# Performance work log

Hardware: AMD Instinct MI355X
Metric: run time of the kernel (lower is better)

Reference implementation:

```python
import jax, jax.numpy as jnp
import numpy as np

B, P, ENC, DEC, ATT, EMB, V, MEM, TCAP = 64, 196, 2048, 512, 512, 512, 10000, 128, 22
T = TCAP - 1  # max decode length (caption_lengths - 1)


def setup_inputs() -> dict:
    key = jax.random.key(0)
    ks = iter(jax.random.split(key, 32))
    def w(shape, s=0.02):
        return (jax.random.normal(next(ks), shape, jnp.float32) * s)
    encoder_out = jax.random.normal(next(ks), (B, P, ENC), jnp.float32)
    encoded_captions = jax.random.randint(next(ks), (B, TCAP), 0, V)
    lens = np.sort(np.asarray(jax.random.randint(next(ks), (B,), 5, TCAP + 1)))[::-1].copy()
    lens[0] = TCAP  # ensure max(decode_lengths) == T
    caption_lengths = jnp.asarray(lens, jnp.int32)
    return {
        'encoder_out': encoder_out,
        'encoded_captions': encoded_captions,
        'caption_lengths': caption_lengths,
        'emb_table': w((V, EMB), 0.05),
        # Linear weights stored as [in, out] (torch W.T), so y = x @ W + b
        'W_enc': w((ENC, ATT)), 'b_enc': jnp.zeros((ATT,), jnp.float32),
        'W_dec': w((DEC, ATT)), 'b_dec': jnp.zeros((ATT,), jnp.float32),
        'W_full': w((ATT, 1)), 'b_full': jnp.zeros((1,), jnp.float32),
        'W_inith': w((ENC, DEC)), 'b_inith': jnp.zeros((DEC,), jnp.float32),
        'W_initc': w((ENC, DEC)), 'b_initc': jnp.zeros((DEC,), jnp.float32),
        'W_beta': w((DEC, ENC)), 'b_beta': jnp.zeros((ENC,), jnp.float32),
        # LSTMCell (torch gate order i, f, g, o), stored as [in, 4*dec]
        'W_ih': w((EMB + ENC, 4 * DEC)), 'b_ih': jnp.zeros((4 * DEC,), jnp.float32),
        'W_hh': w((DEC, 4 * DEC)), 'b_hh': jnp.zeros((4 * DEC,), jnp.float32),
        'memory_bank': jax.random.normal(next(ks), (MEM, DEC), jnp.float32),
        'W_fc': w((DEC, V)), 'b_fc': jnp.zeros((V,), jnp.float32),
    }


def _decode(encoder_out, encoded_captions, caption_lengths, emb_table,
            W_enc, b_enc, W_dec, b_dec, W_full, b_full,
            W_inith, b_inith, W_initc, b_initc, W_beta, b_beta,
            W_ih, b_ih, W_hh, b_hh, memory_bank, W_fc, b_fc):
    dec_len = caption_lengths - 1  # decode_lengths
    embs = emb_table[encoded_captions]                 # [B, TCAP, EMB]
    mean_enc = encoder_out.mean(axis=1)                # [B, ENC]
    h0 = mean_enc @ W_inith + b_inith
    c0 = mean_enc @ W_initc + b_initc
    att1 = encoder_out @ W_enc + b_enc                 # [B, P, ATT] precomputed

    x_seq = jnp.swapaxes(embs[:, :T, :], 0, 1)         # [T, B, EMB]
    mask_seq = jnp.arange(T)[:, None] < dec_len[None, :]  # [T, B]

    def step(carry, inp):
        h, c = carry
        x_t, m = inp                                   # [B,EMB], [B]
        # attention
        att2 = h @ W_dec + b_dec                       # [B, ATT]
        e = (jax.nn.relu(att1 + att2[:, None, :]) @ W_full)[..., 0] + b_full[0]  # [B, P]
        alpha = jax.nn.softmax(e, axis=1)
        awe = jnp.einsum('bpe,bp->be', encoder_out, alpha)  # [B, ENC]
        gate = jax.nn.sigmoid(h @ W_beta + b_beta)
        awe = gate * awe
        # LSTMCell
        xi = jnp.concatenate([x_t, awe], axis=1)
        gates = xi @ W_ih + b_ih + h @ W_hh + b_hh      # [B, 4*DEC]
        gi, gf, gg, go = jnp.split(gates, 4, axis=1)
        c_new = jax.nn.sigmoid(gf) * c + jax.nn.sigmoid(gi) * jnp.tanh(gg)
        h_new = jax.nn.sigmoid(go) * jnp.tanh(c_new)
        # hash memory
        sim = h_new @ memory_bank.T                    # [B, MEM]
        h_new = h_new + jax.nn.softmax(sim, axis=1) @ memory_bank
        # fc (dropout = identity in eval)
        preds = h_new @ W_fc + b_fc                    # [B, V]
        m2 = m[:, None]
        h = jnp.where(m2, h_new, h)
        c = jnp.where(m2, c_new, c)
        preds = jnp.where(m2, preds, 0.0)
        alpha = jnp.where(m2, alpha, 0.0)
        return (h, c), (preds, alpha)

    (_, _), (preds_seq, alpha_seq) = jax.lax.scan(step, (h0, c0), (x_seq, mask_seq))
    predictions = jnp.swapaxes(preds_seq, 0, 1)        # [B, T, V]
    alphas = jnp.swapaxes(alpha_seq, 0, 1)             # [B, T, P]
    return predictions, dec_len, alphas


def reference(encoder_out, encoded_captions, caption_lengths, emb_table,
              W_enc, b_enc, W_dec, b_dec, W_full, b_full,
              W_inith, b_inith, W_initc, b_initc, W_beta, b_beta,
              W_ih, b_ih, W_hh, b_hh, memory_bank, W_fc, b_fc):
    return _decode(encoder_out, encoded_captions, caption_lengths, emb_table,
                   W_enc, b_enc, W_dec, b_dec, W_full, b_full,
                   W_inith, b_inith, W_initc, b_initc, W_beta, b_beta,
                   W_ih, b_ih, W_hh, b_hh, memory_bank, W_fc, b_fc)
```

## Files before the change

### kernel.cpp

```cpp
#include <hip/hip_runtime.h>

#define BB   64
#define PP   196
#define ENCD 2048
#define DECD 512
#define VV   10000
#define TT   21
#define KIH  2560

typedef __attribute__((ext_vector_type(8))) short bf16x8;
typedef __attribute__((ext_vector_type(4))) float f32x4;
typedef float f32x2 __attribute__((ext_vector_type(2)));

__device__ __forceinline__ float sigm(float x)   { return 1.f / (1.f + __expf(-x)); }
__device__ __forceinline__ float tanh_f(float x) { return 1.f - 2.f / (1.f + __expf(2.f * x)); }
__device__ __forceinline__ ushort f2bf(float x) {
    unsigned u = __float_as_uint(x);
    unsigned r = (u + 0x7FFFu + ((u >> 16) & 1u)) >> 16;
    return (ushort)r;
}
__device__ __forceinline__ float bf2f(ushort u) {
    return __uint_as_float(((unsigned)u) << 16);
}
union U8 { float4 f4; ushort u[8]; };

#if __has_builtin(__builtin_amdgcn_cvt_pk_fp8_f32) && __has_builtin(__builtin_amdgcn_cvt_pk_f32_fp8)
#define HAVE_HW_FP8 1
#endif

__device__ uint enc8m(float x) {
    uint s = (__float_as_uint(x) >> 31) << 7;
    float ax = fabsf(x);
    if (!(ax > 0.f)) return s;
    if (ax >= 448.f) return s | 0x7e;
    int e; float m = frexpf(ax, &e);
    int E = e - 1 + 7;
    if (E <= 0) { int q = (int)rintf(ax * 512.f); if (q > 7) return s | 0x08; return s | (uint)q; }
    int q = (int)rintf((m * 2.f - 1.f) * 8.f);
    if (q == 8) { q = 0; ++E; if (E > 15) return s | 0x7e; }
    return s | ((uint)E << 3) | (uint)q;
}
__device__ __forceinline__ float dec8m(uint b) {
    uint s = b >> 7, e = (b >> 3) & 15, m = b & 7;
    float v = (e == 0) ? (float)m * (1.f / 512.f) : ldexpf(1.f + (float)m * 0.125f, (int)e - 7);
    return s ? -v : v;
}
__device__ __forceinline__ uint pkfp8x4(float a, float b, float c, float d) {
#ifdef HAVE_HW_FP8
    int v = __builtin_amdgcn_cvt_pk_fp8_f32(a, b, 0, false);
    v = __builtin_amdgcn_cvt_pk_fp8_f32(c, d, v, true);
    return (uint)v;
#else
    return enc8m(a) | (enc8m(b) << 8) | (enc8m(c) << 16) | (enc8m(d) << 24);
#endif
}
__device__ __forceinline__ void dec8x4(uint v, float out[4]) {
#ifdef HAVE_HW_FP8
    f32x2 lo = __builtin_amdgcn_cvt_pk_f32_fp8((int)v, false);
    f32x2 hi = __builtin_amdgcn_cvt_pk_f32_fp8((int)v, true);
    out[0] = lo[0]; out[1] = lo[1]; out[2] = hi[0]; out[3] = hi[1];
#else
    out[0] = dec8m(v & 255); out[1] = dec8m((v >> 8) & 255);
    out[2] = dec8m((v >> 16) & 255); out[3] = dec8m(v >> 24);
#endif
}


__global__ void k_cvt(const float* __restrict__ in, ushort* __restrict__ out, int n4) {
    int i = blockIdx.x * 256 + threadIdx.x;
    if (i >= n4) return;
    float4 v = ((const float4*)in)[i];
    ushort4 o; o.x = f2bf(v.x); o.y = f2bf(v.y); o.z = f2bf(v.z); o.w = f2bf(v.w);
    ((ushort4*)out)[i] = o;
}

__global__ void k_cvt8(const float* __restrict__ in, uint* __restrict__ out, int n4) {
    int i = blockIdx.x * 256 + threadIdx.x;
    if (i >= n4) return;
    float4 v = ((const float4*)in)[i];
    out[i] = pkfp8x4(v.x, v.y, v.z, v.w);
}

__global__ void k_mean16(const ushort* __restrict__ encB, float* __restrict__ mean) {
    int idx = blockIdx.x * 256 + threadIdx.x;
    int b = idx >> 10, e2 = idx & 1023;
    const uint* p = (const uint*)encB + (size_t)b * PP * 1024 + e2;
    float s0 = 0.f, s1 = 0.f;
    #pragma unroll 7
    for (int i = 0; i < PP; ++i) {
        uint v = p[(size_t)i * 1024];
        s0 += __uint_as_float(v << 16);
        s1 += __uint_as_float(v & 0xffff0000u);
    }
    mean[b * 2048 + e2 * 2]     = s0 * (1.f / 196.f);
    mean[b * 2048 + e2 * 2 + 1] = s1 * (1.f / 196.f);
}

__global__ __launch_bounds__(256) void k_ipart(const float* __restrict__ mean,
        const float* __restrict__ Wh, const float* __restrict__ Wc,
        float* __restrict__ ipart) {
    __shared__ alignas(16) float As[32][68];
    __shared__ alignas(16) float Bs[32][68];
    const int n0 = blockIdx.x * 64;
    const int kc = blockIdx.y;
    const int mat = blockIdx.z;
    const float* Bp = mat ? Wc : Wh;
    const int tid = threadIdx.x, tx = tid & 15, ty = tid >> 4;
    float acc[4][4] = {};
    for (int k0 = 0; k0 < 512; k0 += 32) {
        #pragma unroll
        for (int p = 0; p < 2; ++p) {
            int c = p * 256 + tid;
            int m = c >> 3, k4 = (c & 7) * 4;
            float4 v = *(const float4*)(mean + m * 2048 + kc * 512 + k0 + k4);
            As[k4 + 0][m] = v.x; As[k4 + 1][m] = v.y; As[k4 + 2][m] = v.z; As[k4 + 3][m] = v.w;
            int kb = c >> 4, n4 = (c & 15) * 4;
            float4 w = *(const float4*)(Bp + (size_t)(kc * 512 + k0 + kb) * 512 + n0 + n4);
            *(float4*)&Bs[kb][n4] = w;
        }
        __syncthreads();
        #pragma unroll 8
        for (int k = 0; k < 32; ++k) {
            float4 a = *(const float4*)&As[k][ty * 4];
            float4 b = *(const float4*)&Bs[k][tx * 4];
            float av[4] = {a.x, a.y, a.z, a.w}, bv[4] = {b.x, b.y, b.z, b.w};
            #pragma unroll
            for (int i = 0; i < 4; ++i)
                #pragma unroll
                for (int j = 0; j < 4; ++j) acc[i][j] += av[i] * bv[j];
        }
        __syncthreads();
    }
    #pragma unroll
    for (int i = 0; i < 4; ++i) {
        int m = ty * 4 + i;
        #pragma unroll
        for (int j = 0; j < 4; ++j) {
            int n = n0 + tx * 4 + j;
            ipart[((size_t)(mat * 4 + kc) * BB + m) * 512 + n] = acc[i][j];
        }
    }
}

__global__ void k_ifin(const float* __restrict__ ipart,
                       const float* __restrict__ bh, const float* __restrict__ bc,
                       float* __restrict__ h, float* __restrict__ c, ushort* __restrict__ hB) {
    int idx = blockIdx.x * 256 + threadIdx.x;
    int mat = idx >> 15, rem = idx & 32767;
    int b = rem >> 9, d = rem & 511;
    float s = 0.f;
    #pragma unroll
    for (int kc = 0; kc < 4; ++kc) s += ipart[((size_t)(mat * 4 + kc) * BB + b) * 512 + d];
    if (mat) c[rem] = s + bc[d];
    else { float v = s + bh[d]; h[rem] = v; hB[rem] = f2bf(v); }
}

__global__ __launch_bounds__(256) void k_tcvt_all(
        const float* __restrict__ Wenc, const float* __restrict__ Wdec,
        const float* __restrict__ Wbeta, const float* __restrict__ Whh,
        const float* __restrict__ Wih, const float* __restrict__ Wfc,
        ushort* __restrict__ WencT, ushort* __restrict__ WdecT,
        ushort* __restrict__ WbetaT, ushort* __restrict__ WhhT,
        ushort* __restrict__ WihT, ushort* __restrict__ WfcT) {
    __shared__ float lds[64 * 65];
    int l = blockIdx.x;
    const float* in; ushort* out; int K, N, KT;
    if (l < 256)       { in = Wenc;  out = WencT;  K = 2048; N = 512;   KT = 32; }
    else if (l < 320)  { l -= 256;  in = Wdec;  out = WdecT;  K = 512;  N = 512;   KT = 8; }
    else if (l < 576)  { l -= 320;  in = Wbeta; out = WbetaT; K = 512;  N = 2048;  KT = 8; }
    else if (l < 832)  { l -= 576;  in = Whh;   out = WhhT;   K = 512;  N = 2048;  KT = 8; }
    else if (l < 2112) { l -= 832;  in = Wih;   out = WihT;   K = KIH;  N = 2048;  KT = 40; }
    else               { l -= 2112; in = Wfc;   out = WfcT;   K = 512;  N = 10000; KT = 8; }
    const int k0 = (l % KT) * 64, n0 = (l / KT) * 64;
    const int tid = threadIdx.x;
    for (int i = tid; i < 4096; i += 256) {
        int kk = i >> 6, nn = i & 63;
        float v = 0.f;
        if (n0 + nn < N) v = in[(size_t)(k0 + kk) * N + n0 + nn];
        lds[nn * 65 + kk] = v;
    }
    __syncthreads();
    for (int i = tid; i < 4096; i += 256) {
        int nn = i >> 6, kk = i & 63;
        out[(size_t)(n0 + nn) * K + k0 + kk] = f2bf(lds[nn * 65 + kk]);
    }
}

__global__ __launch_bounds__(256) void k_att1n(const ushort* __restrict__ A,
        const ushort* __restrict__ Bt, const float* __restrict__ bias,
        ushort* __restrict__ C) {
    __shared__ alignas(16) ushort As[64 * 64];
    __shared__ alignas(16) ushort Bs[256 * 64];
    const int n0 = blockIdx.x * 256;
    const int m0 = blockIdx.y * 64;
    const int tid = threadIdx.x, wid = tid >> 6, lane = tid & 63;
    f32x4 acc[4][4] = {};
    for (int k0 = 0; k0 < 2048; k0 += 64) {
        #pragma unroll
        for (int p = 0; p < 2; ++p) {
            int c = p * 256 + tid;
            int r = c >> 3, cc = c & 7;
            float4 v = *(const float4*)(A + (size_t)(m0 + r) * 2048 + k0 + cc * 8);
            *(float4*)(As + r * 64 + ((cc ^ (r & 7)) * 8)) = v;
        }
        #pragma unroll
        for (int p = 0; p < 8; ++p) {
            int c = p * 256 + tid;
            int r = c >> 3, cc = c & 7;
            float4 v = *(const float4*)(Bt + (size_t)(n0 + r) * 2048 + k0 + cc * 8);
            *(float4*)(Bs + r * 64 + ((cc ^ (r & 7)) * 8)) = v;
        }
        __syncthreads();
        #pragma unroll
        for (int kk = 0; kk < 2; ++kk) {
            int ci = kk * 4 + (lane >> 4);
            bf16x8 afrag[4], bfrag[4];
            #pragma unroll
            for (int m = 0; m < 4; ++m) {
                int row = m * 16 + (lane & 15);
                afrag[m] = *(const bf16x8*)(As + row * 64 + ((ci ^ (row & 7)) * 8));
            }
            #pragma unroll
            for (int n = 0; n < 4; ++n) {
                int col = wid * 64 + n * 16 + (lane & 15);
                bfrag[n] = *(const bf16x8*)(Bs + col * 64 + ((ci ^ (col & 7)) * 8));
            }
            #pragma unroll
            for (int m = 0; m < 4; ++m)
                #pragma unroll
                for (int n = 0; n < 4; ++n)
                    acc[m][n] = __builtin_amdgcn_mfma_f32_16x16x32_bf16(afrag[m], bfrag[n], acc[m][n], 0, 0, 0);
        }
        __syncthreads();
    }
    #pragma unroll
    for (int m = 0; m < 4; ++m) {
        int rb = m0 + m * 16 + (lane >> 4) * 4;
        #pragma unroll
        for (int n = 0; n < 4; ++n) {
            int col = n0 + wid * 64 + n * 16 + (lane & 15);
            float bv = bias[col];
            #pragma unroll
            for (int r = 0; r < 4; ++r)
                C[(size_t)(rb + r) * 512 + col] = f2bf(acc[m][n][r] + bv);
        }
    }
}

__global__ __launch_bounds__(256) void k_xpre(const float* __restrict__ emb,
        const int* __restrict__ caps, const ushort* __restrict__ WihT,
        float* __restrict__ xpre) {
    __shared__ alignas(16) ushort As[64 * 64];
    __shared__ alignas(16) ushort Bs[256 * 64];
    __shared__ int capsh[64];
    const int n0 = blockIdx.x * 256;
    const int t = blockIdx.y;
    const int tid = threadIdx.x, wid = tid >> 6, lane = tid & 63;
    if (tid < 64) capsh[tid] = caps[tid * 22 + t];
    __syncthreads();
    f32x4 acc[4][4] = {};
    for (int k0 = 0; k0 < 512; k0 += 64) {
        #pragma unroll
        for (int p = 0; p < 2; ++p) {
            int c = p * 256 + tid;
            int r = c >> 3, cc = c & 7;
            const float* er = emb + (size_t)capsh[r] * 512 + k0 + cc * 8;
            float4 v0 = *(const float4*)er;
            float4 v1 = *(const float4*)(er + 4);
            U8 pk;
            pk.u[0] = f2bf(v0.x); pk.u[1] = f2bf(v0.y); pk.u[2] = f2bf(v0.z); pk.u[3] = f2bf(v0.w);
            pk.u[4] = f2bf(v1.x); pk.u[5] = f2bf(v1.y); pk.u[6] = f2bf(v1.z); pk.u[7] = f2bf(v1.w);
            *(float4*)(As + r * 64 + ((cc ^ (r & 7)) * 8)) = pk.f4;
        }
        #pragma unroll
        for (int p = 0; p < 8; ++p) {
            int c = p * 256 + tid;
            int r = c >> 3, cc = c & 7;
            float4 v = *(const float4*)(WihT + (size_t)(n0 + r) * KIH + k0 + cc * 8);
            *(float4*)(Bs + r * 64 + ((cc ^ (r & 7)) * 8)) = v;
        }
        __syncthreads();
        #pragma unroll
        for (int kk = 0; kk < 2; ++kk) {
            int ci = kk * 4 + (lane >> 4);
            bf16x8 afrag[4], bfrag[4];
            #pragma unroll
            for (int m = 0; m < 4; ++m) {
                int row = m * 16 + (lane & 15);
                afrag[m] = *(const bf16x8*)(As + row * 64 + ((ci ^ (row & 7)) * 8));
            }
            #pragma unroll
            for (int n = 0; n < 4; ++n) {
                int col = wid * 64 + n * 16 + (lane & 15);
                bfrag[n] = *(const bf16x8*)(Bs + col * 64 + ((ci ^ (col & 7)) * 8));
            }
            #pragma unroll
            for (int m = 0; m < 4; ++m)
                #pragma unroll
                for (int n = 0; n < 4; ++n)
                    acc[m][n] = __builtin_amdgcn_mfma_f32_16x16x32_bf16(afrag[m], bfrag[n], acc[m][n], 0, 0, 0);
        }
        __syncthreads();
    }
    #pragma unroll
    for (int m = 0; m < 4; ++m) {
        int rb = m * 16 + (lane >> 4) * 4;
        #pragma unroll
        for (int n = 0; n < 4; ++n) {
            int col = n0 + wid * 64 + n * 16 + (lane & 15);
            #pragma unroll
            for (int r = 0; r < 4; ++r)
                xpre[((size_t)t * BB + rb + r) * 2048 + col] = acc[m][n][r];
        }
    }
}

__global__ void k_declen(const int* __restrict__ lens, float* __restrict__ out) {
    int b = threadIdx.x;
    if (b < BB) out[b] = (float)(lens[b] - 1);
}


__global__ __launch_bounds__(256) void k_p1(const ushort* __restrict__ hB,
        const ushort* __restrict__ WcatT, const float* __restrict__ bd,
        const float* __restrict__ bb, float* __restrict__ att2,
        float* __restrict__ gate, float* __restrict__ hhp) {
    __shared__ alignas(16) ushort As[64 * 64];
    __shared__ alignas(16) ushort Bs[64 * 64];
    const int tid = threadIdx.x, lane = tid & 63, wid = tid >> 6;
    const int n0 = blockIdx.x * 64;
    f32x4 acc[4] = {};
    for (int k0 = 0; k0 < 512; k0 += 64) {
        #pragma unroll
        for (int p = 0; p < 2; ++p) {
            int c8 = p * 256 + tid;
            int r = c8 >> 3, cc = c8 & 7;
            float4 v = *(const float4*)(hB + r * 512 + k0 + cc * 8);
            *(float4*)(As + r * 64 + ((cc ^ (r & 7)) * 8)) = v;
            float4 w = *(const float4*)(WcatT + (size_t)(n0 + r) * 512 + k0 + cc * 8);
            *(float4*)(Bs + r * 64 + ((cc ^ (r & 7)) * 8)) = w;
        }
        __syncthreads();
        #pragma unroll
        for (int kk = 0; kk < 2; ++kk) {
            int ci = kk * 4 + (lane >> 4);
            int colL = wid * 16 + (lane & 15);
            bf16x8 bfrag = *(const bf16x8*)(Bs + colL * 64 + ((ci ^ (colL & 7)) * 8));
            #pragma unroll
            for (int m = 0; m < 4; ++m) {
                int row = m * 16 + (lane & 15);
                bf16x8 afrag = *(const bf16x8*)(As + row * 64 + ((ci ^ (row & 7)) * 8));
                acc[m] = __builtin_amdgcn_mfma_f32_16x16x32_bf16(afrag, bfrag, acc[m], 0, 0, 0);
            }
        }
        __syncthreads();
    }
    int col = n0 + wid * 16 + (lane & 15);
    #pragma unroll
    for (int m = 0; m < 4; ++m) {
        int rb = m * 16 + (lane >> 4) * 4;
        #pragma unroll
        for (int r = 0; r < 4; ++r) {
            int row = rb + r;
            float v = acc[m][r];
            if (col < 512)       att2[row * 512 + col] = v + bd[col];
            else if (col < 2560) gate[row * 2048 + (col - 512)] = sigm(v + bb[col - 512]);
            else                 hhp[(size_t)row * 2048 + (col - 2560)] = v;
        }
    }
}

__global__ __launch_bounds__(256) void k_escore_p(const ushort* __restrict__ att1B,
        const float* __restrict__ att2, const float* __restrict__ Wf,
        float* __restrict__ es) {
    __shared__ float a2[512], wf[512];
    int b = blockIdx.y, pc = blockIdx.x, tid = threadIdx.x;
    for (int i = tid; i < 512; i += 256) { a2[i] = att2[b * 512 + i]; wf[i] = Wf[i]; }
    __syncthreads();
    int lane = tid & 63, wid = tid >> 6;
    for (int i = wid; i < 49; i += 4) {
        int p = pc * 49 + i;
        bf16x8 rv = *(const bf16x8*)(att1B + ((size_t)(b * PP + p)) * 512 + lane * 8);
        float s = 0.f;
        #pragma unroll
        for (int j = 0; j < 8; ++j) {
            float v = bf2f((ushort)rv[j]) + a2[lane * 8 + j];
            s += (v > 0.f ? v : 0.f) * wf[lane * 8 + j];
        }
        #pragma unroll
        for (int off = 32; off; off >>= 1) s += __shfl_down(s, off);
        if (lane == 0) es[b * 256 + p] = s;
    }
}

__global__ __launch_bounds__(256) void k_awe8(const uint* __restrict__ enc8,
        const float* __restrict__ es, const float* __restrict__ gate,
        const int* __restrict__ lens, int t,
        uint* __restrict__ aweB, float* __restrict__ alpha_out) {
    __shared__ float al[224], red[256], ps[4][64][4];
    int b = blockIdx.y, ec = blockIdx.x, tid = threadIdx.x;
    float v = (tid < PP) ? es[b * 256 + tid] : -3.4e38f;
    red[tid] = v; __syncthreads();
    for (int s = 128; s; s >>= 1) { if (tid < s) red[tid] = fmaxf(red[tid], red[tid + s]); __syncthreads(); }
    float mx = red[0]; __syncthreads();
    float ev = (tid < PP) ? __expf(v - mx) : 0.f;
    red[tid] = ev; __syncthreads();
    for (int s = 128; s; s >>= 1) { if (tid < s) red[tid] += red[tid + s]; __syncthreads(); }
    float inv = 1.f / red[0];
    if (tid < PP) {
        float a = ev * inv;
        al[tid] = a;
        if (ec == 0) {
            bool m = t < (lens[b] - 1);
            alpha_out[((size_t)b * TT + t) * PP + tid] = m ? a : 0.f;
        }
    }
    __syncthreads();
    int w = tid >> 6, lane = tid & 63;
    int quad = ec * 64 + lane;
    const uint* pp = enc8 + (size_t)b * PP * 512 + quad;
    float s0 = 0.f, s1 = 0.f, s2 = 0.f, s3 = 0.f;
    #pragma unroll 7
    for (int p = w; p < PP; p += 4) {
        uint vv = pp[(size_t)p * 512];
        float d[4]; dec8x4(vv, d);
        float a = al[p];
        s0 += a * d[0]; s1 += a * d[1]; s2 += a * d[2]; s3 += a * d[3];
    }
    ps[w][lane][0] = s0; ps[w][lane][1] = s1; ps[w][lane][2] = s2; ps[w][lane][3] = s3;
    __syncthreads();
    if (tid < 64) {
        float t0 = ps[0][tid][0] + ps[1][tid][0] + ps[2][tid][0] + ps[3][tid][0];
        float t1 = ps[0][tid][1] + ps[1][tid][1] + ps[2][tid][1] + ps[3][tid][1];
        float t2 = ps[0][tid][2] + ps[1][tid][2] + ps[2][tid][2] + ps[3][tid][2];
        float t3 = ps[0][tid][3] + ps[1][tid][3] + ps[2][tid][3] + ps[3][tid][3];
        int q2 = ec * 64 + tid;
        int e = q2 * 4;
        float g0 = t0 * gate[b * 2048 + e + 0];
        float g1 = t1 * gate[b * 2048 + e + 1];
        float g2 = t2 * gate[b * 2048 + e + 2];
        float g3 = t3 * gate[b * 2048 + e + 3];
        aweB[b * 1024 + q2 * 2]     = (uint)f2bf(g0) | ((uint)f2bf(g1) << 16);
        aweB[b * 1024 + q2 * 2 + 1] = (uint)f2bf(g2) | ((uint)f2bf(g3) << 16);
    }
}

__global__ __launch_bounds__(256) void k_p3(const uint* __restrict__ aweB,
        const ushort* __restrict__ WihT, float* __restrict__ pawe) {
    __shared__ alignas(16) ushort As[64 * 64];
    __shared__ alignas(16) ushort Bs[64 * 64];
    const int tid = threadIdx.x, lane = tid & 63, wid = tid >> 6;
    const int n0 = (blockIdx.x & 31) * 64, kc = blockIdx.x >> 5;
    const ushort* aweU = (const ushort*)aweB;
    f32x4 acc[4] = {};
    for (int k0 = 0; k0 < 512; k0 += 64) {
        #pragma unroll
        for (int p = 0; p < 2; ++p) {
            int c8 = p * 256 + tid;
            int r = c8 >> 3, cc = c8 & 7;
            float4 v = *(const float4*)(aweU + r * 2048 + kc * 512 + k0 + cc * 8);
            *(float4*)(As + r * 64 + ((cc ^ (r & 7)) * 8)) = v;
            float4 w = *(const float4*)(WihT + (size_t)(n0 + r) * KIH + 512 + kc * 512 + k0 + cc * 8);
            *(float4*)(Bs + r * 64 + ((cc ^ (r & 7)) * 8)) = w;
        }
        __syncthreads();
        #pragma unroll
        for (int kk = 0; kk < 2; ++kk) {
            int ci = kk * 4 + (lane >> 4);
            int colL = wid * 16 + (lane & 15);
            bf16x8 bfrag = *(const bf16x8*)(Bs + colL * 64 + ((ci ^ (colL & 7)) * 8));
            #pragma unroll
            for (int m = 0; m < 4; ++m) {
                int row = m * 16 + (lane & 15);
                bf16x8 afrag = *(const bf16x8*)(As + row * 64 + ((ci ^ (row & 7)) * 8));
                acc[m] = __builtin_amdgcn_mfma_f32_16x16x32_bf16(afrag, bfrag, acc[m], 0, 0, 0);
            }
        }
        __syncthreads();
    }
    int col = n0 + wid * 16 + (lane & 15);
    #pragma unroll
    for (int m = 0; m < 4; ++m) {
        int rb = m * 16 + (lane >> 4) * 4;
        #pragma unroll
        for (int r = 0; r < 4; ++r)
            pawe[((size_t)kc * BB + rb + r) * 2048 + col] = acc[m][r];
    }
}

__global__ __launch_bounds__(256) void k_p4(const float* __restrict__ hhp,
        const float* __restrict__ pawe, const float* __restrict__ xpre,
        const float* __restrict__ bih, const float* __restrict__ bhh,
        const int* __restrict__ lens, int t, const float* __restrict__ memB,
        float* __restrict__ h, float* __restrict__ c,
        ushort* __restrict__ hB, ushort* __restrict__ histB) {
    __shared__ float hss[512], simss[128], reds[256], pss[128];
    const int b = blockIdx.x, tid = threadIdx.x;
    const int lane = tid & 63, wid = tid >> 6;
    bool msk = t < (lens[b] - 1);
    for (int j = tid; j < 512; j += 256) {
        float g[4];
        #pragma unroll
        for (int q = 0; q < 4; ++q) {
            int col = q * 512 + j;
            float s = bih[col] + bhh[col]
                    + hhp[(size_t)b * 2048 + col]
                    + xpre[((size_t)t * BB + b) * 2048 + col];
            #pragma unroll
            for (int kc = 0; kc < 4; ++kc) s += pawe[((size_t)kc * BB + b) * 2048 + col];
            g[q] = s;
        }
        float gi = sigm(g[0]), gf = sigm(g[1]), gg = tanh_f(g[2]), go = sigm(g[3]);
        float cold = c[b * 512 + j];
        float cn = gf * cold + gi * gg;
        c[b * 512 + j] = msk ? cn : cold;
        hss[j] = go * tanh_f(cn);
    }
    __syncthreads();
    for (int m = wid * 32; m < wid * 32 + 32; ++m) {
        const float* r = memB + (size_t)m * 512 + lane * 8;
        float4 r0 = *(const float4*)(r);
        float4 r1 = *(const float4*)(r + 4);
        float4 h0 = *(const float4*)(&hss[lane * 8]);
        float4 h1 = *(const float4*)(&hss[lane * 8 + 4]);
        float s = r0.x * h0.x + r0.y * h0.y + r0.z * h0.z + r0.w * h0.w
                + r1.x * h1.x + r1.y * h1.y + r1.z * h1.z + r1.w * h1.w;
        #pragma unroll
        for (int off = 32; off; off >>= 1) s += __shfl_down(s, off);
        if (lane == 0) simss[m] = s;
    }
    __syncthreads();
    float v = (tid < 128) ? simss[tid] : -3.4e38f;
    reds[tid] = v; __syncthreads();
    for (int s = 128; s; s >>= 1) { if (tid < s) reds[tid] = fmaxf(reds[tid], reds[tid + s]); __syncthreads(); }
    float mx = reds[0]; __syncthreads();
    float ev = (tid < 128) ? __expf(v - mx) : 0.f;
    reds[tid] = ev; __syncthreads();
    for (int s = 128; s; s >>= 1) { if (tid < s) reds[tid] += reds[tid + s]; __syncthreads(); }
    if (tid < 128) pss[tid] = ev / reds[0];
    __syncthreads();
    for (int d = tid; d < 512; d += 256) {
        float s = 0.f;
        #pragma unroll 4
        for (int m = 0; m < 128; ++m) s += pss[m] * memB[(size_t)m * 512 + d];
        float hn = hss[d] + s;
        histB[((size_t)t * BB + b) * 512 + d] = f2bf(hn);
        float hold = h[b * 512 + d];
        float hv = msk ? hn : hold;
        h[b * 512 + d] = hv;
        hB[b * 512 + d] = f2bf(hv);
    }
}

__global__ __launch_bounds__(256) void k_preds_batch(const ushort* __restrict__ histB,
        const ushort* __restrict__ WfcT, const float* __restrict__ bfc,
        const int* __restrict__ lens, float* __restrict__ out) {
    __shared__ alignas(16) ushort As[64 * 64];
    __shared__ alignas(16) ushort Bs[256 * 64];
    const int n0 = blockIdx.x * 256;
    const int t = blockIdx.y;
    const ushort* A = histB + (size_t)t * BB * 512;
    const int tid = threadIdx.x, wid = tid >> 6, lane = tid & 63;
    f32x4 acc[4][4] = {};
    for (int k0 = 0; k0 < 512; k0 += 64) {
        #pragma unroll
        for (int p = 0; p < 2; ++p) {
            int c = p * 256 + tid;
            int r = c >> 3, cc = c & 7;
            float4 v = *(const float4*)(A + r * 512 + k0 + cc * 8);
            *(float4*)(As + r * 64 + ((cc ^ (r & 7)) * 8)) = v;
        }
        #pragma unroll
        for (int p = 0; p < 8; ++p) {
            int c = p * 256 + tid;
            int r = c >> 3, cc = c & 7;
            float4 v = *(const float4*)(WfcT + (size_t)(n0 + r) * 512 + k0 + cc * 8);
            *(float4*)(Bs + r * 64 + ((cc ^ (r & 7)) * 8)) = v;
        }
        __syncthreads();
        #pragma unroll
        for (int kk = 0; kk < 2; ++kk) {
            int ci = kk * 4 + (lane >> 4);
            bf16x8 afrag[4], bfrag[4];
            #pragma unroll
            for (int m = 0; m < 4; ++m) {
                int row = m * 16 + (lane & 15);
                afrag[m] = *(const bf16x8*)(As + row * 64 + ((ci ^ (row & 7)) * 8));
            }
            #pragma unroll
            for (int n = 0; n < 4; ++n) {
                int col = wid * 64 + n * 16 + (lane & 15);
                bfrag[n] = *(const bf16x8*)(Bs + col * 64 + ((ci ^ (col & 7)) * 8));
            }
            #pragma unroll
            for (int m = 0; m < 4; ++m)
                #pragma unroll
                for (int n = 0; n < 4; ++n)
                    acc[m][n] = __builtin_amdgcn_mfma_f32_16x16x32_bf16(afrag[m], bfrag[n], acc[m][n], 0, 0, 0);
        }
        __syncthreads();
    }
    #pragma unroll
    for (int m = 0; m < 4; ++m) {
        int rb = m * 16 + (lane >> 4) * 4;
        #pragma unroll
        for (int n = 0; n < 4; ++n) {
            int col = n0 + wid * 64 + n * 16 + (lane & 15);
            if (col < VV) {
                float bv = bfc[col];
                #pragma unroll
                for (int r = 0; r < 4; ++r) {
                    int b = rb + r;
                    bool msk = t < (lens[b] - 1);
                    out[((size_t)b * TT + t) * VV + col] = msk ? (acc[m][n][r] + bv) : 0.f;
                }
            }
        }
    }
}


extern "C" void kernel_launch(void* const* d_in, const int* in_sizes, int n_in,
                              void* d_out, int out_size, void* d_ws, size_t ws_size,
                              hipStream_t stream) {
    const float* enc     = (const float*)d_in[0];
    const int*   caps    = (const int*)d_in[1];
    const int*   lens    = (const int*)d_in[2];
    const float* emb     = (const float*)d_in[3];
    const float* W_enc   = (const float*)d_in[4];
    const float* b_enc   = (const float*)d_in[5];
    const float* W_dec   = (const float*)d_in[6];
    const float* b_dec   = (const float*)d_in[7];
    const float* W_full  = (const float*)d_in[8];
    const float* W_inith = (const float*)d_in[10];
    const float* b_inith = (const float*)d_in[11];
    const float* W_initc = (const float*)d_in[12];
    const float* b_initc = (const float*)d_in[13];
    const float* W_beta  = (const float*)d_in[14];
    const float* b_beta  = (const float*)d_in[15];
    const float* W_ih    = (const float*)d_in[16];
    const float* b_ih    = (const float*)d_in[17];
    const float* W_hh    = (const float*)d_in[18];
    const float* b_hh    = (const float*)d_in[19];
    const float* memB    = (const float*)d_in[20];
    const float* W_fc    = (const float*)d_in[21];
    const float* b_fc    = (const float*)d_in[22];

    float* out = (float*)d_out;
    float* preds_out  = out;
    float* declen_out = out + (size_t)BB * TT * VV;
    float* alpha_out  = declen_out + BB;

    float* ws    = (float*)d_ws;
    ushort* att1B = (ushort*)ws;  ws += (size_t)12544 * 512 / 2;
    float* h     = ws;  ws += BB * DECD;
    float* c     = ws;  ws += BB * DECD;
    float* att2  = ws;  ws += BB * 512;
    float* gate  = ws;  ws += BB * 2048;
    float* hhp   = ws;  ws += BB * 2048;
    float* es    = ws;  ws += BB * 256;
    float* pawe  = ws;  ws += (size_t)4 * BB * 2048;
    float* xpre  = ws;  ws += (size_t)TT * BB * 2048;
    ushort* hB   = (ushort*)ws;  ws += BB * DECD / 2;
    uint*  aweB  = (uint*)ws;    ws += BB * 1024;
    ushort* histB = (ushort*)ws; ws += (size_t)TT * BB * DECD / 2;
    ushort* encB  = (ushort*)ws; ws += (size_t)12544 * 2048 / 2;
    ushort* WencT = (ushort*)ws; ws += (size_t)512 * 2048 / 2;
    ushort* WfcT  = (ushort*)ws; ws += (size_t)10240 * 512 / 2;
    ushort* WcatT = (ushort*)ws; ws += (size_t)4608 * 512 / 2;
    ushort* WihT  = (ushort*)ws; ws += (size_t)2048 * KIH / 2;
    float* mean  = (float*)att1B;
    float* ipart = xpre;
    uint*  enc8  = (uint*)encB;

    k_cvt<<<(12544 * 2048 / 4 + 255) / 256, 256, 0, stream>>>(enc, encB, 12544 * 2048 / 4);
    k_mean16<<<256, 256, 0, stream>>>(encB, mean);
    k_ipart<<<dim3(8, 4, 2), 256, 0, stream>>>(mean, W_inith, W_initc, ipart);
    k_ifin<<<256, 256, 0, stream>>>(ipart, b_inith, b_initc, h, c, hB);
    k_declen<<<1, 64, 0, stream>>>(lens, declen_out);
    k_tcvt_all<<<3392, 256, 0, stream>>>(W_enc, W_dec, W_beta, W_hh, W_ih, W_fc,
                                         WencT, WcatT, WcatT + (size_t)512 * 512,
                                         WcatT + (size_t)2560 * 512, WihT, WfcT);
    k_att1n<<<dim3(2, 196), 256, 0, stream>>>(encB, WencT, b_enc, att1B);
    k_cvt8<<<(12544 * 2048 / 4 + 255) / 256, 256, 0, stream>>>(enc, enc8, 12544 * 2048 / 4);
    k_xpre<<<dim3(8, TT), 256, 0, stream>>>(emb, caps, WihT, xpre);

    for (int t = 0; t < TT; ++t) {
        k_p1<<<72, 256, 0, stream>>>(hB, WcatT, b_dec, b_beta, att2, gate, hhp);
        k_escore_p<<<dim3(4, 64), 256, 0, stream>>>(att1B, att2, W_full, es);
        k_awe8<<<dim3(8, 64), 256, 0, stream>>>(enc8, es, gate, lens, t, aweB, alpha_out);
        k_p3<<<128, 256, 0, stream>>>(aweB, WihT, pawe);
        k_p4<<<64, 256, 0, stream>>>(hhp, pawe, xpre, b_ih, b_hh, lens, t, memB, h, c, hB, histB);
    }

    k_preds_batch<<<dim3(40, TT), 256, 0, stream>>>(histB, WfcT, b_fc, lens, preds_out);
}
```

Baseline: 1.664 ms.

## Fuse attention score and weighted-encoding kernels; merge bf16/fp8 conversion passes

Merges the per-step score kernel and the softmax/attention-weighted-encoding kernel into one kernel with one block per batch row, keeping scores in shared memory instead of a global buffer. This removes one launch per decode step and the redundant per-block softmax recomputation. It also merges the bf16 and fp8 conversion of encoder_out into one pass that reads the input once, which requires giving the fp8 copy its own workspace instead of aliasing the bf16 buffer. The trade-off is that the per-step grid drops from 512 blocks to 64, so each block streams its whole fp8 encoder slice serially, which may underuse the GPU's compute units.

```diff
diff --git a/kernel.cpp b/kernel.cpp
--- a/kernel.cpp
+++ b/kernel.cpp
@@ -66,19 +66,14 @@
 }
 
 
-__global__ void k_cvt(const float* __restrict__ in, ushort* __restrict__ out, int n4) {
+__global__ void k_cvt2(const float* __restrict__ in, ushort* __restrict__ outB,
+                       uint* __restrict__ out8, int n4) {
     int i = blockIdx.x * 256 + threadIdx.x;
     if (i >= n4) return;
     float4 v = ((const float4*)in)[i];
     ushort4 o; o.x = f2bf(v.x); o.y = f2bf(v.y); o.z = f2bf(v.z); o.w = f2bf(v.w);
-    ((ushort4*)out)[i] = o;
-}
-
-__global__ void k_cvt8(const float* __restrict__ in, uint* __restrict__ out, int n4) {
-    int i = blockIdx.x * 256 + threadIdx.x;
-    if (i >= n4) return;
-    float4 v = ((const float4*)in)[i];
-    out[i] = pkfp8x4(v.x, v.y, v.z, v.w);
+    ((ushort4*)outB)[i] = o;
+    out8[i] = pkfp8x4(v.x, v.y, v.z, v.w);
 }
 
 __global__ void k_mean16(const ushort* __restrict__ encB, float* __restrict__ mean) {
@@ -370,16 +365,17 @@
     }
 }
 
-__global__ __launch_bounds__(256) void k_escore_p(const ushort* __restrict__ att1B,
+__global__ __launch_bounds__(256) void k_esawe(const ushort* __restrict__ att1B,
         const float* __restrict__ att2, const float* __restrict__ Wf,
-        float* __restrict__ es) {
-    __shared__ float a2[512], wf[512];
-    int b = blockIdx.y, pc = blockIdx.x, tid = threadIdx.x;
+        const uint* __restrict__ enc8, const float* __restrict__ gate,
+        const int* __restrict__ lens, int t,
+        uint* __restrict__ aweB, float* __restrict__ alpha_out) {
+    __shared__ float a2[512], wf[512], als[224], red[256];
+    const int b = blockIdx.x, tid = threadIdx.x;
+    const int lane = tid & 63, wid = tid >> 6;
     for (int i = tid; i < 512; i += 256) { a2[i] = att2[b * 512 + i]; wf[i] = Wf[i]; }
     __syncthreads();
-    int lane = tid & 63, wid = tid >> 6;
-    for (int i = wid; i < 49; i += 4) {
-        int p = pc * 49 + i;
+    for (int p = wid; p < PP; p += 4) {
         bf16x8 rv = *(const bf16x8*)(att1B + ((size_t)(b * PP + p)) * 512 + lane * 8);
         float s = 0.f;
         #pragma unroll
@@ -389,17 +385,10 @@
         }
         #pragma unroll
         for (int off = 32; off; off >>= 1) s += __shfl_down(s, off);
-        if (lane == 0) es[b * 256 + p] = s;
-    }
-}
-
-__global__ __launch_bounds__(256) void k_awe8(const uint* __restrict__ enc8,
-        const float* __restrict__ es, const float* __restrict__ gate,
-        const int* __restrict__ lens, int t,
-        uint* __restrict__ aweB, float* __restrict__ alpha_out) {
-    __shared__ float al[224], red[256], ps[4][64][4];
-    int b = blockIdx.y, ec = blockIdx.x, tid = threadIdx.x;
-    float v = (tid < PP) ? es[b * 256 + tid] : -3.4e38f;
+        if (lane == 0) als[p] = s;
+    }
+    __syncthreads();
+    float v = (tid < PP) ? als[tid] : -3.4e38f;
     red[tid] = v; __syncthreads();
     for (int s = 128; s; s >>= 1) { if (tid < s) red[tid] = fmaxf(red[tid], red[tid + s]); __syncthreads(); }
     float mx = red[0]; __syncthreads();
@@ -409,39 +398,40 @@
     float inv = 1.f / red[0];
     if (tid < PP) {
         float a = ev * inv;
-        al[tid] = a;
-        if (ec == 0) {
-            bool m = t < (lens[b] - 1);
-            alpha_out[((size_t)b * TT + t) * PP + tid] = m ? a : 0.f;
-        }
-    }
-    __syncthreads();
-    int w = tid >> 6, lane = tid & 63;
-    int quad = ec * 64 + lane;
-    const uint* pp = enc8 + (size_t)b * PP * 512 + quad;
+        als[tid] = a;
+        bool m = t < (lens[b] - 1);
+        alpha_out[((size_t)b * TT + t) * PP + tid] = m ? a : 0.f;
+    }
+    __syncthreads();
+    const uint* pp = enc8 + (size_t)b * PP * 512;
     float s0 = 0.f, s1 = 0.f, s2 = 0.f, s3 = 0.f;
-    #pragma unroll 7
-    for (int p = w; p < PP; p += 4) {
-        uint vv = pp[(size_t)p * 512];
-        float d[4]; dec8x4(vv, d);
-        float a = al[p];
-        s0 += a * d[0]; s1 += a * d[1]; s2 += a * d[2]; s3 += a * d[3];
-    }
-    ps[w][lane][0] = s0; ps[w][lane][1] = s1; ps[w][lane][2] = s2; ps[w][lane][3] = s3;
-    __syncthreads();
-    if (tid < 64) {
-        float t0 = ps[0][tid][0] + ps[1][tid][0] + ps[2][tid][0] + ps[3][tid][0];
-        float t1 = ps[0][tid][1] + ps[1][tid][1] + ps[2][tid][1] + ps[3][tid][1];
-        float t2 = ps[0][tid][2] + ps[1][tid][2] + ps[2][tid][2] + ps[3][tid][2];
-        float t3 = ps[0][tid][3] + ps[1][tid][3] + ps[2][tid][3] + ps[3][tid][3];
-        int q2 = ec * 64 + tid;
-        int e = q2 * 4;
-        float g0 = t0 * gate[b * 2048 + e + 0];
-        float g1 = t1 * gate[b * 2048 + e + 1];
-        float g2 = t2 * gate[b * 2048 + e + 2];
-        float g3 = t3 * gate[b * 2048 + e + 3];
-        aweB[b * 1024 + q2 * 2]     = (uint)f2bf(g0) | ((uint)f2bf(g1) << 16);
-        aweB[b * 1024 + q2 * 2 + 1] = (uint)f2bf(g2) | ((uint)f2bf(g3) << 16);
+    float r0 = 0.f, r1 = 0.f, r2 = 0.f, r3 = 0.f;
+    #pragma unroll 4
+    for (int p = 0; p < PP; ++p) {
+        uint va = pp[(size_t)p * 512 + tid];
+        uint vb = pp[(size_t)p * 512 + tid + 256];
+        float a = als[p];
+        float da[4], db[4];
+        dec8x4(va, da); dec8x4(vb, db);
+        s0 += a * da[0]; s1 += a * da[1]; s2 += a * da[2]; s3 += a * da[3];
+        r0 += a * db[0]; r1 += a * db[1]; r2 += a * db[2]; r3 += a * db[3];
+    }
+    {
+        int e = tid * 4;
+        float g0 = s0 * gate[b * 2048 + e + 0];
+        float g1 = s1 * gate[b * 2048 + e + 1];
+        float g2 = s2 * gate[b * 2048 + e + 2];
+        float g3 = s3 * gate[b * 2048 + e + 3];
+        aweB[b * 1024 + tid * 2]     = (uint)f2bf(g0) | ((uint)f2bf(g1) << 16);
+        aweB[b * 1024 + tid * 2 + 1] = (uint)f2bf(g2) | ((uint)f2bf(g3) << 16);
+        int q2 = tid + 256;
+        int e2 = q2 * 4;
+        float h0 = r0 * gate[b * 2048 + e2 + 0];
+        float h1 = r1 * gate[b * 2048 + e2 + 1];
+        float h2 = r2 * gate[b * 2048 + e2 + 2];
+        float h3 = r3 * gate[b * 2048 + e2 + 3];
+        aweB[b * 1024 + q2 * 2]     = (uint)f2bf(h0) | ((uint)f2bf(h1) << 16);
+        aweB[b * 1024 + q2 * 2 + 1] = (uint)f2bf(h2) | ((uint)f2bf(h3) << 16);
     }
 }
 
@@ -658,22 +648,21 @@
     float* att2  = ws;  ws += BB * 512;
     float* gate  = ws;  ws += BB * 2048;
     float* hhp   = ws;  ws += BB * 2048;
-    float* es    = ws;  ws += BB * 256;
     float* pawe  = ws;  ws += (size_t)4 * BB * 2048;
     float* xpre  = ws;  ws += (size_t)TT * BB * 2048;
     ushort* hB   = (ushort*)ws;  ws += BB * DECD / 2;
     uint*  aweB  = (uint*)ws;    ws += BB * 1024;
     ushort* histB = (ushort*)ws; ws += (size_t)TT * BB * DECD / 2;
     ushort* encB  = (ushort*)ws; ws += (size_t)12544 * 2048 / 2;
+    uint*  enc8  = (uint*)ws;    ws += (size_t)12544 * 2048 / 4;
     ushort* WencT = (ushort*)ws; ws += (size_t)512 * 2048 / 2;
     ushort* WfcT  = (ushort*)ws; ws += (size_t)10240 * 512 / 2;
     ushort* WcatT = (ushort*)ws; ws += (size_t)4608 * 512 / 2;
     ushort* WihT  = (ushort*)ws; ws += (size_t)2048 * KIH / 2;
     float* mean  = (float*)att1B;
     float* ipart = xpre;
-    uint*  enc8  = (uint*)encB;
-
-    k_cvt<<<(12544 * 2048 / 4 + 255) / 256, 256, 0, stream>>>(enc, encB, 12544 * 2048 / 4);
+
+    k_cvt2<<<(12544 * 2048 / 4 + 255) / 256, 256, 0, stream>>>(enc, encB, enc8, 12544 * 2048 / 4);
     k_mean16<<<256, 256, 0, stream>>>(encB, mean);
     k_ipart<<<dim3(8, 4, 2), 256, 0, stream>>>(mean, W_inith, W_initc, ipart);
     k_ifin<<<256, 256, 0, stream>>>(ipart, b_inith, b_initc, h, c, hB);
@@ -682,13 +671,11 @@
                                          WencT, WcatT, WcatT + (size_t)512 * 512,
                                          WcatT + (size_t)2560 * 512, WihT, WfcT);
     k_att1n<<<dim3(2, 196), 256, 0, stream>>>(encB, WencT, b_enc, att1B);
-    k_cvt8<<<(12544 * 2048 / 4 + 255) / 256, 256, 0, stream>>>(enc, enc8, 12544 * 2048 / 4);
     k_xpre<<<dim3(8, TT), 256, 0, stream>>>(emb, caps, WihT, xpre);
 
     for (int t = 0; t < TT; ++t) {
         k_p1<<<72, 256, 0, stream>>>(hB, WcatT, b_dec, b_beta, att2, gate, hhp);
-        k_escore_p<<<dim3(4, 64), 256, 0, stream>>>(att1B, att2, W_full, es);
-        k_awe8<<<dim3(8, 64), 256, 0, stream>>>(enc8, es, gate, lens, t, aweB, alpha_out);
+        k_esawe<<<64, 256, 0, stream>>>(att1B, att2, W_full, enc8, gate, lens, t, aweB, alpha_out);
         k_p3<<<128, 256, 0, stream>>>(aweB, WihT, pawe);
         k_p4<<<64, 256, 0, stream>>>(hhp, pawe, xpre, b_ih, b_hh, lens, t, memB, h, c, hB, histB);
     }
```

Result: slower. 2.330 ms (+40.0%).
